# Optimization experiments

Hardware: AMD Instinct MI355X
Metric: run time of the kernel (lower is better)

Reference implementation:

```python
import jax, jax.numpy as jnp
import numpy as np
import math

E = 16          # num_experts
TOP_K = 2       # num_experts_per_tok (used as capacity_factor in EC routing)
D = 1024        # embed_dim
F = 4096        # expert_hidden_dim = mlp_ratio * D
SH = 2048       # shared intermediate = F * n_shared_experts // mlp_ratio


def setup_inputs() -> dict:
    key = jax.random.key(0)
    ks = jax.random.split(key, 10)
    s = lambda k, shape, fan: jax.random.normal(k, shape, jnp.float32) / np.sqrt(fan)
    return {
        "x": jax.random.normal(ks[0], (32, 256, D), jnp.float32),
        "gate_w": s(ks[1], (E, D), D),                 # ECMoEGate.weight
        "up_w": s(ks[2], (E, F, D), D),                # fused_up.weight
        "up_b": s(ks[3], (E, F), D),                   # fused_up.bias
        "gw": s(ks[4], (E, F, D), D),                  # fused_gate.weight
        "gb": s(ks[5], (E, F), D),                     # fused_gate.bias
        "down_w": s(ks[6], (E, D, F), F),              # fused_down.weight
        "down_b": s(ks[7], (E, D), F),                 # fused_down.bias
        "sh_gate_w": s(ks[8], (SH, D), D),             # shared_experts.gate_proj
        "sh_up_w": s(ks[9], (SH, D), D),               # shared_experts.up_proj
        "sh_down_w": s(jax.random.fold_in(key, 11), (D, SH), SH),  # shared_experts.down_proj
    }


def reference(x, gate_w, up_w, up_b, gw, gb, down_w, down_b, sh_gate_w, sh_up_w, sh_down_w):
    B, S, Dm = x.shape
    h = x.reshape(-1, Dm)                               # [T, D]
    T = h.shape[0]
    # gate: sigmoid scores, expert-choice top-k over tokens per expert
    scores = jax.nn.sigmoid(h @ gate_w.T)               # [T, E]
    cap = math.ceil(T / E * TOP_K)                      # capacity per expert
    topk_score, topk_ids = jax.lax.top_k(scores.T, cap) # [E, cap]
    # dispatch: gather tokens per expert
    xin = h[topk_ids]                                   # [E, cap, D]
    # batched expert GLU (baddbmm equivalent)
    up = jnp.einsum('ecd,efd->ecf', xin, up_w) + up_b[:, None, :]
    g = jnp.einsum('ecd,efd->ecf', xin, gw) + gb[:, None, :]
    eo = jax.nn.silu(g) * up                            # [E, cap, F]
    eo = jnp.einsum('ecf,edf->ecd', eo, down_w) + down_b[:, None, :]
    # combine: weighted scatter-add back to token positions
    flat = (eo * topk_score[..., None]).reshape(-1, Dm) # [E*cap, D]
    out = jnp.zeros_like(h).at[topk_ids.reshape(-1)].add(flat)
    out = out.reshape(B, S, Dm)
    # shared dense GLU MLP (SiLU)
    shared = (jax.nn.silu(jnp.einsum('bsd,fd->bsf', x, sh_gate_w))
              * jnp.einsum('bsd,fd->bsf', x, sh_up_w))
    shared = jnp.einsum('bsf,df->bsd', shared, sh_down_w)
    return out + shared
```

## Files before the change

kernel.cpp:

```cpp
#include <hip/hip_runtime.h>
#include <hip/hip_bf16.h>

#define Tn 8192
#define Dn 1024
#define Fn 4096
#define SHn 2048
#define En 16
#define CAPn 1024

typedef __bf16 bf16_t;
typedef bf16_t bf16x8 __attribute__((ext_vector_type(8)));
typedef float f32x4 __attribute__((ext_vector_type(4)));

__device__ __forceinline__ unsigned short f2bf(float f) {
  unsigned int u = __builtin_bit_cast(unsigned int, f);
  u += 0x7FFFu + ((u >> 16) & 1u);
  return (unsigned short)(u >> 16);
}
__device__ __forceinline__ unsigned int pack2(float a, float b) {
  return (unsigned int)f2bf(a) | ((unsigned int)f2bf(b) << 16);
}

__device__ __forceinline__ void gload16(const void* g, void* l) {
  __builtin_amdgcn_global_load_lds(
      (const __attribute__((address_space(1))) unsigned int*)g,
      (__attribute__((address_space(3))) unsigned int*)l, 16, 0, 0);
}

__device__ __forceinline__ void conv_blocks(int cb, int ncb, int tid,
                                            const float* s1, unsigned short* d1, int n1,
                                            const float* s2, unsigned short* d2, int n2) {
  const int tot = n1 + n2;
  for (int i = cb * 256 + tid; i < tot; i += ncb * 256) {
    const float4* sv; uint4* dv; int j;
    if (i < n1) { j = i; sv = (const float4*)s1; dv = (uint4*)d1; }
    else        { j = i - n1; sv = (const float4*)s2; dv = (uint4*)d2; }
    float4 a = sv[2 * j], b = sv[2 * j + 1];
    dv[j] = uint4{ pack2(a.x, a.y), pack2(a.z, a.w), pack2(b.x, b.y), pack2(b.z, b.w) };
  }
}

__global__ __launch_bounds__(256) void kscores_cvt(
    const float* __restrict__ x, const float* __restrict__ gw,
    float* __restrict__ sc, unsigned short* __restrict__ xb,
    const float* __restrict__ shg, unsigned short* __restrict__ shgb,
    const float* __restrict__ shu, unsigned short* __restrict__ shub,
    const float* __restrict__ shd, unsigned short* __restrict__ shdb) {
  __shared__ float sx[Dn];
  const int tid = threadIdx.x;
  if (blockIdx.x >= Tn) {
    const int cb = blockIdx.x - Tn, ncb = gridDim.x - Tn;
    constexpr int nsh = SHn * Dn / 8;
    conv_blocks(cb, ncb, tid, shg, shgb, nsh, shu, shub, nsh);
    conv_blocks(cb, ncb, tid, shd, shdb, nsh, nullptr, nullptr, 0);
    return;
  }
  const int tok = blockIdx.x;
  float4 v = ((const float4*)(x + (size_t)tok * Dn))[tid];
  ((float4*)sx)[tid] = v;
  ((uint2*)(xb + (size_t)tok * Dn))[tid] = uint2{ pack2(v.x, v.y), pack2(v.z, v.w) };
  __syncthreads();
  int e = tid >> 4, kl = tid & 15;
  const float4* w = (const float4*)(gw + e * Dn);
  const float4* xv = (const float4*)sx;
  float acc = 0.f;
#pragma unroll
  for (int j = 0; j < 16; ++j) {
    float4 a = w[kl + 16 * j], b = xv[kl + 16 * j];
    acc += a.x * b.x + a.y * b.y + a.z * b.z + a.w * b.w;
  }
#pragma unroll
  for (int off = 8; off; off >>= 1) acc += __shfl_xor(acc, off, 64);
  if (kl == 0) sc[(size_t)e * Tn + tok] = 1.f / (1.f + expf(-acc));
}

__global__ __launch_bounds__(256) void kselect(const float* __restrict__ scores,
                                               int* __restrict__ ids,
                                               float* __restrict__ oscore) {
  __shared__ unsigned int keys[Tn];
  __shared__ unsigned int hist[256];
  __shared__ unsigned int sh_prefix, sh_k, sh_cnt, sh_eq;
  __shared__ int eqlist[1024];
  const int tid = threadIdx.x, e = blockIdx.x;
  const float* row = scores + (size_t)e * Tn;
  for (int i = 0; i < Tn / 256; ++i)
    keys[tid + i * 256] = __float_as_uint(row[tid + i * 256]);
  if (tid == 0) { sh_prefix = 0u; sh_k = CAPn; }
  __syncthreads();
  for (int shift = 24; shift >= 0; shift -= 8) {
    hist[tid] = 0u;
    __syncthreads();
    unsigned int prefix = sh_prefix;
    unsigned int mask = (shift == 24) ? 0u : (0xFFFFFFFFu << (shift + 8));
    for (int i = 0; i < Tn / 256; ++i) {
      unsigned int kk = keys[tid + i * 256];
      if ((kk & mask) == prefix) atomicAdd(&hist[(kk >> shift) & 255], 1u);
    }
    __syncthreads();
    if (tid == 0) {
      unsigned int k = sh_k, c = 0; int b;
      for (b = 255; b >= 0; --b) { c += hist[b]; if (c >= k) break; }
      sh_k = k - (c - hist[b]);
      sh_prefix = prefix | ((unsigned int)b << shift);
    }
    __syncthreads();
  }
  const unsigned int thr = sh_prefix;
  if (tid == 0) { sh_cnt = 0u; sh_eq = 0u; }
  __syncthreads();
  const int base = e * CAPn;
  for (int i = 0; i < Tn / 256; ++i) {
    int t = tid + i * 256;
    unsigned int kk = keys[t];
    if (kk > thr) {
      unsigned int p = atomicAdd(&sh_cnt, 1u);
      ids[base + p] = t;
      oscore[base + p] = __uint_as_float(kk);
    } else if (kk == thr) {
      unsigned int p = atomicAdd(&sh_eq, 1u);
      if (p < 1024u) eqlist[p] = t;
    }
  }
  __syncthreads();
  if (tid == 0) {
    int need = CAPn - (int)sh_cnt;
    int m = (int)sh_eq; if (m > 1024) m = 1024;
    for (int j = 0; j < need; ++j) {
      int best = 1 << 30, bi = 0;
      for (int i2 = 0; i2 < m; ++i2)
        if (eqlist[i2] < best) { best = eqlist[i2]; bi = i2; }
      eqlist[bi] = 1 << 30;
      ids[base + (int)sh_cnt + j] = best;
      oscore[base + (int)sh_cnt + j] = __uint_as_float(thr);
    }
  }
}


template <bool GATHER>
__global__ __launch_bounds__(256, 2) void kglu_bf(
    const unsigned short* __restrict__ X, const int* __restrict__ idsg,
    const unsigned short* __restrict__ Wg, const unsigned short* __restrict__ Wu,
    const float* __restrict__ biasg, const float* __restrict__ biasu,
    unsigned short* __restrict__ H, int N, int Mz, int MB, int NB,
    int gemmN,
    const float* __restrict__ cS1, unsigned short* __restrict__ cD1, int cn1,
    const float* __restrict__ cS2, unsigned short* __restrict__ cD2, int cn2) {
  constexpr int K = Dn;
  __shared__ alignas(16) unsigned char sA[16384];
  __shared__ alignas(16) unsigned char sB1[16384];
  __shared__ alignas(16) unsigned char sB2[16384];
  __shared__ int sIds[128];
  const int tid = threadIdx.x;
  const int bid = blockIdx.x;
  if (bid >= gemmN) {
    conv_blocks(bid - gemmN, gridDim.x - gemmN, tid, cS1, cD1, cn1, cS2, cD2, cn2);
    return;
  }
  const int cpx = gemmN >> 3;
  const int swz = (bid & 7) * cpx + (bid >> 3);
  const int bm = swz % MB;
  const int bn = (swz / MB) % NB;
  const int z  = swz / (MB * NB);
  const int lane = tid & 63, w = tid >> 6;
  const int wm = w >> 1, wn = w & 1;
  const int lrow = lane & 15, lk = lane >> 4;
  const int row0 = bm * 128;

  if (tid < 128) sIds[tid] = GATHER ? idsg[z * CAPn + row0 + tid] : (row0 + tid);
  __syncthreads();

  const int lr = lane >> 3;
  const int lc = lane & 7;
  const int srcb = ((lc ^ lr) << 4);
  const unsigned char* Xb = (const unsigned char*)X;
  const unsigned char* Gb = (const unsigned char*)Wg + (size_t)z * N * (K * 2);
  const unsigned char* Ub = (const unsigned char*)Wu + (size_t)z * N * (K * 2);
  const unsigned char* aP[4];
#pragma unroll
  for (int i = 0; i < 4; ++i) {
    int ar = w * 32 + 8 * i + lr;
    aP[i] = Xb + (size_t)sIds[ar] * (K * 2) + srcb;
  }
  const int br0 = bn * 128 + w * 32 + lr;
  const unsigned char* gP0 = Gb + (size_t)br0 * (K * 2) + srcb;
  const unsigned char* uP0 = Ub + (size_t)br0 * (K * 2) + srcb;

  f32x4 accG[4][4], accU[4][4];
#pragma unroll
  for (int m = 0; m < 4; ++m)
#pragma unroll
    for (int n = 0; n < 4; ++n) {
      accG[m][n] = {0.f, 0.f, 0.f, 0.f};
      accU[m][n] = {0.f, 0.f, 0.f, 0.f};
    }

  for (int k0b = 0; k0b < K * 2; k0b += 128) {
    __syncthreads();
#pragma unroll
    for (int i = 0; i < 4; ++i) {
      unsigned ldsoff = (unsigned)(w * 32 + 8 * i) * 128u;
      gload16(aP[i] + k0b, sA + ldsoff);
      gload16(gP0 + (size_t)i * 8 * (K * 2) + k0b, sB1 + ldsoff);
      gload16(uP0 + (size_t)i * 8 * (K * 2) + k0b, sB2 + ldsoff);
    }
    __syncthreads();
#pragma unroll
    for (int ks = 0; ks < 2; ++ks) {
      const int swb = (((ks * 4 + lk) ^ (lrow & 7)) << 4);
      bf16x8 av[4], gv[4], uv[4];
#pragma unroll
      for (int m = 0; m < 4; ++m)
        av[m] = *(const bf16x8*)(sA + (wm * 64 + m * 16 + lrow) * 128 + swb);
#pragma unroll
      for (int n = 0; n < 4; ++n) {
        gv[n] = *(const bf16x8*)(sB1 + (wn * 64 + n * 16 + lrow) * 128 + swb);
        uv[n] = *(const bf16x8*)(sB2 + (wn * 64 + n * 16 + lrow) * 128 + swb);
      }
#pragma unroll
      for (int m = 0; m < 4; ++m)
#pragma unroll
        for (int n = 0; n < 4; ++n) {
          accG[m][n] = __builtin_amdgcn_mfma_f32_16x16x32_bf16(av[m], gv[n], accG[m][n], 0, 0, 0);
          accU[m][n] = __builtin_amdgcn_mfma_f32_16x16x32_bf16(av[m], uv[n], accU[m][n], 0, 0, 0);
        }
    }
  }
#pragma unroll
  for (int n = 0; n < 4; ++n) {
    int col = bn * 128 + wn * 64 + n * 16 + lrow;
    float bg = biasg ? biasg[(size_t)z * N + col] : 0.f;
    float bu = biasu ? biasu[(size_t)z * N + col] : 0.f;
#pragma unroll
    for (int m = 0; m < 4; ++m) {
#pragma unroll
      for (int j = 0; j < 4; ++j) {
        float g = accG[m][n][j] + bg;
        float u = accU[m][n][j] + bu;
        float h = g / (1.f + __expf(-g)) * u;
        int row = row0 + wm * 64 + m * 16 + lk * 4 + j;
        H[(size_t)z * Mz * N + (size_t)row * N + col] = f2bf(h);
      }
    }
  }
}

template <int K, bool SCATTER>
__global__ __launch_bounds__(256, 2) void kdown_bf(
    const unsigned short* __restrict__ Hin, const unsigned short* __restrict__ W,
    const float* __restrict__ bias, const int* __restrict__ idsg,
    const float* __restrict__ scg, float* __restrict__ Out, int Mz, int MB, int NB) {
  constexpr int N = Dn;
  __shared__ alignas(16) unsigned char sA[16384];
  __shared__ alignas(16) unsigned char sB[16384];
  __shared__ int sIds[128];
  __shared__ float sSc[128];
  const int tid = threadIdx.x;
  const int nwg = gridDim.x;
  const int cpx = nwg >> 3;
  const int bid = blockIdx.x;
  const int swz = (bid & 7) * cpx + (bid >> 3);
  const int bm = swz % MB;
  const int bn = (swz / MB) % NB;
  const int z  = swz / (MB * NB);
  const int lane = tid & 63, w = tid >> 6;
  const int wm = w >> 1, wn = w & 1;
  const int lrow = lane & 15, lk = lane >> 4;
  const int row0 = bm * 128;

  if (SCATTER && tid < 128) {
    sIds[tid] = idsg[z * CAPn + row0 + tid];
    sSc[tid] = scg[z * CAPn + row0 + tid];
  }
  __syncthreads();

  const int lr = lane >> 3;
  const int lc = lane & 7;
  const int srcb = ((lc ^ lr) << 4);
  const unsigned char* Ab = (const unsigned char*)Hin + (size_t)z * Mz * (K * 2);
  const unsigned char* Wb = (const unsigned char*)W + (size_t)z * N * (K * 2);
  const int ar0 = row0 + w * 32 + lr;
  const int br0 = bn * 128 + w * 32 + lr;
  const unsigned char* aP0 = Ab + (size_t)ar0 * (K * 2) + srcb;
  const unsigned char* bP0 = Wb + (size_t)br0 * (K * 2) + srcb;

  f32x4 acc[4][4];
#pragma unroll
  for (int m = 0; m < 4; ++m)
#pragma unroll
    for (int n = 0; n < 4; ++n) acc[m][n] = {0.f, 0.f, 0.f, 0.f};

  for (int k0b = 0; k0b < K * 2; k0b += 128) {
    __syncthreads();
#pragma unroll
    for (int i = 0; i < 4; ++i) {
      unsigned ldsoff = (unsigned)(w * 32 + 8 * i) * 128u;
      gload16(aP0 + (size_t)i * 8 * (K * 2) + k0b, sA + ldsoff);
      gload16(bP0 + (size_t)i * 8 * (K * 2) + k0b, sB + ldsoff);
    }
    __syncthreads();
#pragma unroll
    for (int ks = 0; ks < 2; ++ks) {
      const int swb = (((ks * 4 + lk) ^ (lrow & 7)) << 4);
      bf16x8 av[4], bv[4];
#pragma unroll
      for (int m = 0; m < 4; ++m)
        av[m] = *(const bf16x8*)(sA + (wm * 64 + m * 16 + lrow) * 128 + swb);
#pragma unroll
      for (int n = 0; n < 4; ++n)
        bv[n] = *(const bf16x8*)(sB + (wn * 64 + n * 16 + lrow) * 128 + swb);
#pragma unroll
      for (int m = 0; m < 4; ++m)
#pragma unroll
        for (int n = 0; n < 4; ++n)
          acc[m][n] = __builtin_amdgcn_mfma_f32_16x16x32_bf16(av[m], bv[n], acc[m][n], 0, 0, 0);
    }
  }
#pragma unroll
  for (int n = 0; n < 4; ++n) {
    int col = bn * 128 + wn * 64 + n * 16 + lrow;
    float bvv = bias ? bias[(size_t)z * N + col] : 0.f;
#pragma unroll
    for (int m = 0; m < 4; ++m) {
#pragma unroll
      for (int j = 0; j < 4; ++j) {
        int rl = wm * 64 + m * 16 + lk * 4 + j;
        float v = acc[m][n][j] + bvv;
        if (SCATTER) {
          atomicAdd(Out + (size_t)sIds[rl] * Dn + col, sSc[rl] * v);
        } else {
          Out[(size_t)(row0 + rl) * Dn + col] = v;
        }
      }
    }
  }
}

extern "C" void kernel_launch(void* const* d_in, const int* in_sizes, int n_in,
                              void* d_out, int out_size, void* d_ws, size_t ws_size,
                              hipStream_t stream) {
  const float* x      = (const float*)d_in[0];
  const float* gate_w = (const float*)d_in[1];
  const float* up_w   = (const float*)d_in[2];
  const float* up_b   = (const float*)d_in[3];
  const float* gw     = (const float*)d_in[4];
  const float* gb     = (const float*)d_in[5];
  const float* down_w = (const float*)d_in[6];
  const float* down_b = (const float*)d_in[7];
  const float* shg    = (const float*)d_in[8];
  const float* shu    = (const float*)d_in[9];
  const float* shd    = (const float*)d_in[10];
  float* out = (float*)d_out;

  const size_t H_BYTES  = (size_t)En * CAPn * Fn * 2;
  const size_t XB_BYTES = (size_t)Tn * Dn * 2;
  const size_t WE_BYTES = (size_t)En * Fn * Dn * 2;
  const size_t SH_BYTES = (size_t)SHn * Dn * 2;
  const size_t SC_BYTES = (size_t)En * Tn * 4;
  const size_t ID_BYTES = (size_t)En * CAPn * 4;
  const size_t need = H_BYTES + XB_BYTES + 3 * WE_BYTES + 3 * SH_BYTES +
                      SC_BYTES + 2 * ID_BYTES;
  if (ws_size < need) return;

  char* p = (char*)d_ws;
  unsigned short* H    = (unsigned short*)p; p += H_BYTES;
  unsigned short* xb   = (unsigned short*)p; p += XB_BYTES;
  unsigned short* upb  = (unsigned short*)p; p += WE_BYTES;
  unsigned short* gwb  = (unsigned short*)p; p += WE_BYTES;
  unsigned short* dwb  = (unsigned short*)p; p += WE_BYTES;
  unsigned short* shgb = (unsigned short*)p; p += SH_BYTES;
  unsigned short* shub = (unsigned short*)p; p += SH_BYTES;
  unsigned short* shdb = (unsigned short*)p; p += SH_BYTES;
  float* scores = (float*)p; p += SC_BYTES;
  int* ids      = (int*)p;  p += ID_BYTES;
  float* osc    = (float*)p;

  constexpr int NWE8 = En * Fn * Dn / 8;

  kscores_cvt<<<Tn + 256, 256, 0, stream>>>(x, gate_w, scores, xb,
                                            shg, shgb, shu, shub, shd, shdb);
  kselect<<<En, 256, 0, stream>>>(scores, ids, osc);

  kglu_bf<false><<<(Tn / 128) * (SHn / 128) + 2048, 256, 0, stream>>>(
      xb, nullptr, shgb, shub, nullptr, nullptr, H, SHn, Tn, Tn / 128, SHn / 128,
      (Tn / 128) * (SHn / 128), up_w, upb, NWE8, gw, gwb, NWE8);

  kdown_bf<SHn, false><<<(Tn / 128) * (Dn / 128), 256, 0, stream>>>(
      H, shdb, nullptr, nullptr, nullptr, out, Tn, Tn / 128, Dn / 128);

  kglu_bf<true><<<(CAPn / 128) * (Fn / 128) * En + 1024, 256, 0, stream>>>(
      xb, ids, gwb, upb, gb, up_b, H, Fn, CAPn, CAPn / 128, Fn / 128,
      (CAPn / 128) * (Fn / 128) * En, down_w, dwb, NWE8, nullptr, nullptr, 0);

  kdown_bf<Fn, true><<<(CAPn / 128) * (Dn / 128) * En, 256, 0, stream>>>(
      H, dwb, down_b, ids, osc, out, CAPn, CAPn / 128, Dn / 128);
}
```

Before: 967.3 us.

## Interleave weight conversion blocks among GEMM blocks and rebalance across kernels

Conversion of expert weights from fp32 to bf16 is no longer appended as a tail of extra blocks after the GEMM blocks. It is now interleaved as every P-th block, so it runs alongside the GEMM work instead of forming a serialized tail. The gw conversion moves from the shared GLU kernel into the shared down kernel to balance load, and the conversion loop is unrolled by four for more memory-level parallelism. The risk is that GEMM blocks lose some L2 locality and the swizzle mapping becomes more complex.

```diff
diff --git a/kernel.cpp b/kernel.cpp
--- a/kernel.cpp
+++ b/kernel.cpp
@@ -37,6 +37,27 @@
     else        { j = i - n1; sv = (const float4*)s2; dv = (uint4*)d2; }
     float4 a = sv[2 * j], b = sv[2 * j + 1];
     dv[j] = uint4{ pack2(a.x, a.y), pack2(a.z, a.w), pack2(b.x, b.y), pack2(b.z, b.w) };
+  }
+}
+
+__device__ __forceinline__ void conv4(int cb, int ncb, int tid,
+                                      const float* __restrict__ s,
+                                      unsigned short* __restrict__ d, int n8) {
+  const int step = ncb * 256;
+  const float4* sv = (const float4*)s;
+  uint4* dv = (uint4*)d;
+  for (int i = cb * 256 + tid; i < n8; i += 4 * step) {
+    const int i1 = i + step, i2 = i + 2 * step, i3 = i + 3 * step;
+    const bool v1 = i1 < n8, v2 = i2 < n8, v3 = i3 < n8;
+    float4 a0 = sv[2 * i], b0 = sv[2 * i + 1];
+    float4 a1{}, b1{}, a2{}, b2{}, a3{}, b3{};
+    if (v1) { a1 = sv[2 * i1]; b1 = sv[2 * i1 + 1]; }
+    if (v2) { a2 = sv[2 * i2]; b2 = sv[2 * i2 + 1]; }
+    if (v3) { a3 = sv[2 * i3]; b3 = sv[2 * i3 + 1]; }
+    dv[i] = uint4{ pack2(a0.x, a0.y), pack2(a0.z, a0.w), pack2(b0.x, b0.y), pack2(b0.z, b0.w) };
+    if (v1) dv[i1] = uint4{ pack2(a1.x, a1.y), pack2(a1.z, a1.w), pack2(b1.x, b1.y), pack2(b1.z, b1.w) };
+    if (v2) dv[i2] = uint4{ pack2(a2.x, a2.y), pack2(a2.z, a2.w), pack2(b2.x, b2.y), pack2(b2.z, b2.w) };
+    if (v3) dv[i3] = uint4{ pack2(a3.x, a3.y), pack2(a3.z, a3.w), pack2(b3.x, b3.y), pack2(b3.z, b3.w) };
   }
 }
 
@@ -143,9 +164,8 @@
     const unsigned short* __restrict__ Wg, const unsigned short* __restrict__ Wu,
     const float* __restrict__ biasg, const float* __restrict__ biasu,
     unsigned short* __restrict__ H, int N, int Mz, int MB, int NB,
-    int gemmN,
-    const float* __restrict__ cS1, unsigned short* __restrict__ cD1, int cn1,
-    const float* __restrict__ cS2, unsigned short* __restrict__ cD2, int cn2) {
+    int gemmN, int convP,
+    const float* __restrict__ cS1, unsigned short* __restrict__ cD1, int cn1) {
   constexpr int K = Dn;
   __shared__ alignas(16) unsigned char sA[16384];
   __shared__ alignas(16) unsigned char sB1[16384];
@@ -153,12 +173,13 @@
   __shared__ int sIds[128];
   const int tid = threadIdx.x;
   const int bid = blockIdx.x;
-  if (bid >= gemmN) {
-    conv_blocks(bid - gemmN, gridDim.x - gemmN, tid, cS1, cD1, cn1, cS2, cD2, cn2);
+  if (convP && (bid % convP) == convP - 1) {
+    conv4(bid / convP, gridDim.x - gemmN, tid, cS1, cD1, cn1);
     return;
   }
+  const int gbid = convP ? (bid - bid / convP) : bid;
   const int cpx = gemmN >> 3;
-  const int swz = (bid & 7) * cpx + (bid >> 3);
+  const int swz = (gbid & 7) * cpx + (gbid >> 3);
   const int bm = swz % MB;
   const int bn = (swz / MB) % NB;
   const int z  = swz / (MB * NB);
@@ -249,17 +270,23 @@
 __global__ __launch_bounds__(256, 2) void kdown_bf(
     const unsigned short* __restrict__ Hin, const unsigned short* __restrict__ W,
     const float* __restrict__ bias, const int* __restrict__ idsg,
-    const float* __restrict__ scg, float* __restrict__ Out, int Mz, int MB, int NB) {
+    const float* __restrict__ scg, float* __restrict__ Out, int Mz, int MB, int NB,
+    int gemmN, int convP,
+    const float* __restrict__ cS1, unsigned short* __restrict__ cD1, int cn1) {
   constexpr int N = Dn;
   __shared__ alignas(16) unsigned char sA[16384];
   __shared__ alignas(16) unsigned char sB[16384];
   __shared__ int sIds[128];
   __shared__ float sSc[128];
   const int tid = threadIdx.x;
-  const int nwg = gridDim.x;
-  const int cpx = nwg >> 3;
   const int bid = blockIdx.x;
-  const int swz = (bid & 7) * cpx + (bid >> 3);
+  if (convP && (bid % convP) == convP - 1) {
+    conv4(bid / convP, gridDim.x - gemmN, tid, cS1, cD1, cn1);
+    return;
+  }
+  const int gbid = convP ? (bid - bid / convP) : bid;
+  const int cpx = gemmN >> 3;
+  const int swz = (gbid & 7) * cpx + (gbid >> 3);
   const int bm = swz % MB;
   const int bn = (swz / MB) % NB;
   const int z  = swz / (MB * NB);
@@ -381,17 +408,19 @@
                                             shg, shgb, shu, shub, shd, shdb);
   kselect<<<En, 256, 0, stream>>>(scores, ids, osc);
 
-  kglu_bf<false><<<(Tn / 128) * (SHn / 128) + 2048, 256, 0, stream>>>(
+  kglu_bf<false><<<1024 + 1024, 256, 0, stream>>>(
       xb, nullptr, shgb, shub, nullptr, nullptr, H, SHn, Tn, Tn / 128, SHn / 128,
-      (Tn / 128) * (SHn / 128), up_w, upb, NWE8, gw, gwb, NWE8);
-
-  kdown_bf<SHn, false><<<(Tn / 128) * (Dn / 128), 256, 0, stream>>>(
-      H, shdb, nullptr, nullptr, nullptr, out, Tn, Tn / 128, Dn / 128);
-
-  kglu_bf<true><<<(CAPn / 128) * (Fn / 128) * En + 1024, 256, 0, stream>>>(
+      1024, 2, up_w, upb, NWE8);
+
+  kdown_bf<SHn, false><<<512 + 512, 256, 0, stream>>>(
+      H, shdb, nullptr, nullptr, nullptr, out, Tn, Tn / 128, Dn / 128,
+      512, 2, gw, gwb, NWE8);
+
+  kglu_bf<true><<<4096 + 1024, 256, 0, stream>>>(
       xb, ids, gwb, upb, gb, up_b, H, Fn, CAPn, CAPn / 128, Fn / 128,
-      (CAPn / 128) * (Fn / 128) * En, down_w, dwb, NWE8, nullptr, nullptr, 0);
-
-  kdown_bf<Fn, true><<<(CAPn / 128) * (Dn / 128) * En, 256, 0, stream>>>(
-      H, dwb, down_b, ids, osc, out, CAPn, CAPn / 128, Dn / 128);
-}
+      4096, 5, down_w, dwb, NWE8);
+
+  kdown_bf<Fn, true><<<1024, 256, 0, stream>>>(
+      H, dwb, down_b, ids, osc, out, CAPn, CAPn / 128, Dn / 128,
+      1024, 0, nullptr, nullptr, 0);
+}
```

After: 939.8 us. 2.8% less time.
